# Kernel tuning notes

Measured on AMD Instinct MI355X. Metric: run time of the kernel, lower is better.

The kernel has to match this reference:

```python
import jax, jax.numpy as jnp
import numpy as np

# ---- hardware / module constants (match init_kwargs) ----
IN_BITS = 8
OUT_PREC_BITS = 8
OUT_RANGE_BITS = 4
VMAX = 0.6                      # hardware_input_vmax
I_SCALE = 8020.0                # hardware_output_current_scaling
DAC_SCALE = 1.0 / 2 ** (IN_BITS - 1)
DAC_MAX = 2 ** (IN_BITS - 1)
DAC_MIN = -DAC_MAX
ADC_SCALE = 1.0 / 2 ** OUT_PREC_BITS
ADC_MAX = 2 ** (OUT_PREC_BITS + OUT_RANGE_BITS - 1)
ADC_MIN = -ADC_MAX
BW = 1e-08
KBT = 1.380649e-23 * 300.0
E_CONST = float(np.exp(1))
V_EPS = 1e-12                   # noise_minimum_voltage
WP = 3                          # weight_precision -> L = WP-1 bit levels
L = WP - 1
MI, MO = 128, 128               # memristor tile size
TJ, TK = 2, 2                   # input/output tiling (256/128)
OUT_FEATURES = 256


def fake_quant(x, scale, qmin, qmax):
    # torch.fake_quantize_per_tensor_affine with zero_point=0 (STE grads)
    q = jnp.round(x / scale)
    y = jnp.clip(q, qmin, qmax) * scale
    mask = (q >= qmin) & (q <= qmax)
    xg = jnp.where(mask, x, jax.lax.stop_gradient(x))
    return xg + jax.lax.stop_gradient(y - xg)


def poly_eval(c, x):
    # c: [2, P] ascending-degree coeffs (pos/neg stacked), x: [B,T,I] -> [2,B,T,I]
    # Horner form: same math as sum_p c_p * x**p, grad-safe at x == 0.
    acc = jnp.broadcast_to(c[:, -1][:, None, None, None], (2,) + x.shape)
    for p in range(c.shape[-1] - 2, -1, -1):
        acc = acc * x[None] + c[:, p][:, None, None, None]
    return acc


def _paired_array(cl, ch, r, v, noise):
    # cl:[2,Pl] ch:[2,Ph] r:[2,MI,MO] v:[B,T,MI] noise:[2,T,MI,MO]
    low = poly_eval(cl, v)[..., None]       # [2,B,T,MI,1]
    high = poly_eval(ch, v)[..., None]
    r_b = r[:, None, None]                  # [2,1,1,MI,MO]
    raw = low * (1.0 - r_b) + high * r_b    # [2,B,T,MI,MO]
    johnson = 4.0 * KBT * BW * jnp.abs(raw / (jnp.abs(v)[None, ..., None] + V_EPS))
    shot = 2.0 * E_CONST * jnp.abs(raw) * BW
    sigma = jnp.sqrt(johnson + shot)
    noised = raw + noise[:, None] * sigma   # noise broadcast over batch dim B
    out = jnp.sum(noised, axis=-2)          # reduce over I -> [2,B,T,MO]
    return out[0] - out[1]                  # paired (pos - neg) bitlines


def _forward(x, poly_low, poly_high, r, bias):
    v = fake_quant(x, DAC_SCALE, DAC_MIN, DAC_MAX) * VMAX   # DAC
    B, T, _ = x.shape
    out = jnp.zeros((B, T, TK * MO), x.dtype)
    for i, bit in enumerate(reversed(range(WP - 1))):
        for j in range(TJ):
            vj = v[..., j * MI:(j + 1) * MI]
            for k in range(TK):
                nkey = jax.random.fold_in(jax.random.key(42), i * TJ * TK + j * TK + k)
                noise = jax.random.normal(nkey, (2, T, MI, MO), x.dtype)
                pair = _paired_array(poly_low[i, j, k], poly_high[i, j, k], r[i, j, k], vj, noise)
                adc_out = fake_quant(pair * I_SCALE, ADC_SCALE, ADC_MIN, ADC_MAX)  # ADC
                out = out.at[..., k * MO:(k + 1) * MO].add(adc_out * (2.0 ** bit))
    return out[..., :OUT_FEATURES] + bias


def setup_inputs() -> dict:
    key = jax.random.key(0)
    ks = jax.random.split(key, 5)
    x = jax.random.normal(ks[0], (4, 256, 256), jnp.float32)
    poly_low = jax.random.normal(ks[1], (L, TJ, TK, 2, 7), jnp.float32) * 1e-3
    poly_high = jax.random.normal(ks[2], (L, TJ, TK, 2, 6), jnp.float32) * 1e-3
    r = jax.random.uniform(ks[3], (L, TJ, TK, 2, MI, MO), dtype=jnp.float32)
    bias = jax.random.normal(ks[4], (OUT_FEATURES,), jnp.float32) * 0.01
    return {"x": x, "poly_low": poly_low, "poly_high": poly_high, "r": r, "bias": bias}


def reference(x, poly_low, poly_high, r, bias):
    return _forward(x, poly_low, poly_high, r, bias)
```

## Files before the change

### kernel.cpp

```cpp
#include <hip/hip_runtime.h>
#include <stdint.h>


struct KeyPack { uint32_t k0[8]; uint32_t k1[8]; uint32_t k2[8]; };

#define TFR(r) { x0 += x1; x1 = __builtin_amdgcn_alignbit(x1, x1, 32u - (r)); x1 ^= x0; }

__device__ __forceinline__ uint32_t tf_bits(uint32_t ks0, uint32_t ks1,
                                            uint32_t ks2, uint32_t x1) {
  uint32_t x0 = ks0;
  TFR(13) TFR(15) TFR(26) TFR(6)
  x0 += ks1; x1 += ks2 + 1u;
  TFR(17) TFR(29) TFR(16) TFR(24)
  x0 += ks2; x1 += ks0 + 2u;
  TFR(13) TFR(15) TFR(26) TFR(6)
  x0 += ks0; x1 += ks1 + 3u;
  TFR(17) TFR(29) TFR(16) TFR(24)
  x0 += ks1; x1 += ks2 + 4u;
  TFR(13) TFR(15) TFR(26) TFR(6)
  x0 += ks2; x1 += ks0 + 5u;
  return x0 ^ x1;
}

__host__ __device__ inline void threefry2x32_host(uint32_t k0, uint32_t k1,
                                                  uint32_t x0, uint32_t x1,
                                                  uint32_t& y0, uint32_t& y1) {
  const uint32_t ks0 = k0, ks1 = k1, ks2 = k0 ^ k1 ^ 0x1BD11BDAu;
  x0 += ks0; x1 += ks1;
#define TF_ROUND(r) { x0 += x1; x1 = (x1 << (r)) | (x1 >> (32 - (r))); x1 ^= x0; }
  TF_ROUND(13) TF_ROUND(15) TF_ROUND(26) TF_ROUND(6)
  x0 += ks1; x1 += ks2 + 1u;
  TF_ROUND(17) TF_ROUND(29) TF_ROUND(16) TF_ROUND(24)
  x0 += ks2; x1 += ks0 + 2u;
  TF_ROUND(13) TF_ROUND(15) TF_ROUND(26) TF_ROUND(6)
  x0 += ks0; x1 += ks1 + 3u;
  TF_ROUND(17) TF_ROUND(29) TF_ROUND(16) TF_ROUND(24)
  x0 += ks1; x1 += ks2 + 4u;
  TF_ROUND(13) TF_ROUND(15) TF_ROUND(26) TF_ROUND(6)
  x0 += ks2; x1 += ks0 + 5u;
#undef TF_ROUND
  y0 = x0; y1 = x1;
}

__device__ __forceinline__ float bits_to_normal(uint32_t bits) {
  float g = __uint_as_float(__builtin_amdgcn_alignbit(0x7Fu, bits, 9u));
  float u = fmaxf(fmaf(g, 2.0f, -3.0f), -0.99999994f);
  float w = -__logf(fmaf(u, -u, 1.0f));
  float p;
  if (w < 5.0f) {
    w -= 2.5f;
    p = (float)(2.81022636e-08 * 1.4142135623730951);
    p = fmaf(p, w, (float)( 3.43273939e-07 * 1.4142135623730951));
    p = fmaf(p, w, (float)(-3.5233877e-06  * 1.4142135623730951));
    p = fmaf(p, w, (float)(-4.39150654e-06 * 1.4142135623730951));
    p = fmaf(p, w, (float)( 0.00021858087  * 1.4142135623730951));
    p = fmaf(p, w, (float)(-0.00125372503  * 1.4142135623730951));
    p = fmaf(p, w, (float)(-0.00417768164  * 1.4142135623730951));
    p = fmaf(p, w, (float)( 0.246640727    * 1.4142135623730951));
    p = fmaf(p, w, (float)( 1.50140941     * 1.4142135623730951));
  } else {
    w = __builtin_amdgcn_sqrtf(w) - 3.0f;
    p = (float)(-0.000200214257 * 1.4142135623730951);
    p = fmaf(p, w, (float)( 0.000100950558 * 1.4142135623730951));
    p = fmaf(p, w, (float)( 0.00134934322  * 1.4142135623730951));
    p = fmaf(p, w, (float)(-0.00367342844  * 1.4142135623730951));
    p = fmaf(p, w, (float)( 0.00573950773  * 1.4142135623730951));
    p = fmaf(p, w, (float)(-0.0076224613   * 1.4142135623730951));
    p = fmaf(p, w, (float)( 0.00943887047  * 1.4142135623730951));
    p = fmaf(p, w, (float)( 1.00167406     * 1.4142135623730951));
    p = fmaf(p, w, (float)( 2.83297682     * 1.4142135623730951));
  }
  return p * u;
}

__global__ void memristor_init(const float* __restrict__ bias,
                               float* __restrict__ out) {
  int idx = blockIdx.x * 256 + threadIdx.x;
  out[idx] = bias[idx & 255];
}

__global__ __launch_bounds__(256, 4)
void memristor_main(const float* __restrict__ x,
                    const float* __restrict__ poly_low,
                    const float* __restrict__ poly_high,
                    const float* __restrict__ r,
                    float* __restrict__ out,
                    KeyPack keys) {
  __shared__ __align__(16) float LH[128][16];
  __shared__ float RED[128][9];

  const int tid = threadIdx.x;
  const int bid = blockIdx.x;
  const int c = bid >> 8;
  const int t = bid & 255;
  const int j = (c >> 1) & 1;
  const int k = c & 1;

  for (int task = tid; task < 1024; task += 256) {
    int pb = task & 7;
    int mi = task >> 3;
    int p = pb >> 2, b = pb & 3;
    float xv = x[(b * 256 + t) * 256 + j * 128 + mi];
    float q = rintf(xv * 128.0f);
    q = fminf(fmaxf(q, -128.0f), 128.0f);
    float v = (q * 0.0078125f) * 0.6f;
    const float* cl = poly_low + (c * 2 + p) * 7;
    float lo = cl[6];
    #pragma unroll
    for (int n = 5; n >= 0; --n) lo = fmaf(lo, v, cl[n]);
    const float* ch = poly_high + (c * 2 + p) * 6;
    float hi = ch[5];
    #pragma unroll
    for (int n = 4; n >= 0; --n) hi = fmaf(hi, v, ch[n]);
    LH[mi][pb] = lo;
    LH[mi][8 + pb] = hi - lo;
  }
  __syncthreads();

  const int mo = tid & 127;
  const int mih = tid >> 7;
  const int miBase = mih * 64;
  const uint32_t k0 = keys.k0[c], k1 = keys.k1[c], k2 = keys.k2[c];
  const float* r0p = r + c * 32768 + miBase * 128 + mo;
  const float* r1p = r0p + 16384;
  uint32_t sk = (uint32_t)(t * 16384 + miBase * 128 + mo) + k1;

  float acc[8];
  #pragma unroll
  for (int v2 = 0; v2 < 8; ++v2) acc[v2] = 0.0f;

  const float KS = (float)((double)((float)(2.0 * 2.718281828459045)) *
                           (double)(1e-8f));

  #pragma unroll 2
  for (int ii = 0; ii < 64; ++ii) {
    const float4* lh4 = (const float4*)(&LH[miBase + ii][0]);
    float4 L0 = lh4[0];
    float4 L1 = lh4[1];
    float4 D0 = lh4[2];
    float4 D1 = lh4[3];
    float r0 = r0p[ii * 128];
    float r1 = r1p[ii * 128];

    uint32_t b0 = tf_bits(k0, k1, k2, sk);
    uint32_t b1 = tf_bits(k0, k1, k2, sk + 4194304u);
    float n0 = bits_to_normal(b0);
    float n1 = bits_to_normal(b1);
    sk += 128u;

    float raw0 = fmaf(D0.x, r0, L0.x);
    float raw1 = fmaf(D0.y, r0, L0.y);
    float raw2 = fmaf(D0.z, r0, L0.z);
    float raw3 = fmaf(D0.w, r0, L0.w);
    float raw4 = fmaf(D1.x, r1, L1.x);
    float raw5 = fmaf(D1.y, r1, L1.y);
    float raw6 = fmaf(D1.z, r1, L1.z);
    float raw7 = fmaf(D1.w, r1, L1.w);

    float s0 = __builtin_amdgcn_sqrtf(KS * fabsf(raw0));
    float s1 = __builtin_amdgcn_sqrtf(KS * fabsf(raw1));
    float s2 = __builtin_amdgcn_sqrtf(KS * fabsf(raw2));
    float s3 = __builtin_amdgcn_sqrtf(KS * fabsf(raw3));
    float s4 = __builtin_amdgcn_sqrtf(KS * fabsf(raw4));
    float s5 = __builtin_amdgcn_sqrtf(KS * fabsf(raw5));
    float s6 = __builtin_amdgcn_sqrtf(KS * fabsf(raw6));
    float s7 = __builtin_amdgcn_sqrtf(KS * fabsf(raw7));

    acc[0] += fmaf(n0, s0, raw0);
    acc[1] += fmaf(n0, s1, raw1);
    acc[2] += fmaf(n0, s2, raw2);
    acc[3] += fmaf(n0, s3, raw3);
    acc[4] += fmaf(n1, s4, raw4);
    acc[5] += fmaf(n1, s5, raw5);
    acc[6] += fmaf(n1, s6, raw6);
    acc[7] += fmaf(n1, s7, raw7);
  }

  if (mih == 1) {
    #pragma unroll
    for (int v2 = 0; v2 < 8; ++v2) RED[mo][v2] = acc[v2];
  }
  __syncthreads();
  if (mih == 0) {
    #pragma unroll
    for (int v2 = 0; v2 < 8; ++v2) acc[v2] += RED[mo][v2];
    const float QSC = 2053120.0f;
    const float OSC = (c & 4) ? 0.00390625f : 0.0078125f;
    #pragma unroll
    for (int b = 0; b < 4; ++b) {
      float pair = acc[b] - acc[4 + b];
      float q = rintf(pair * QSC);
      q = fminf(fmaxf(q, -2048.0f), 2048.0f);
      atomicAdd(&out[(b * 256 + t) * 256 + k * 128 + mo], q * OSC);
    }
  }
}

extern "C" void kernel_launch(void* const* d_in, const int* in_sizes, int n_in,
                              void* d_out, int out_size, void* d_ws, size_t ws_size,
                              hipStream_t stream) {
  const float* x    = (const float*)d_in[0];
  const float* pl   = (const float*)d_in[1];
  const float* ph   = (const float*)d_in[2];
  const float* r    = (const float*)d_in[3];
  const float* bias = (const float*)d_in[4];
  float* out = (float*)d_out;

  KeyPack keys;
  for (uint32_t cc = 0; cc < 8; ++cc) {
    uint32_t y0, y1;
    threefry2x32_host(0u, 42u, 0u, cc, y0, y1);
    keys.k0[cc] = y0; keys.k1[cc] = y1;
    keys.k2[cc] = y0 ^ y1 ^ 0x1BD11BDAu;
  }

  memristor_init<<<1024, 256, 0, stream>>>(bias, out);
  memristor_main<<<2048, 256, 0, stream>>>(x, pl, ph, r, out, keys);
}
```

Baseline: 223.5 us.

## Pack FMAs into float2 vectors, fold threefry key injection, software-pipeline loads

Rewrites the inner loop to use two-wide float vectors so the compiler can emit packed FMA/multiply instructions on MI355X. The threefry key-injection adds are folded into the first round's addition, removing a separate add per injection. The loop is restructured to prefetch the next iteration's LDS and r values before computing the current step, to hide memory latency. The risk is higher register pressure and a wasted wraparound prefetch on the last iteration.

```diff
diff --git a/kernel.cpp b/kernel.cpp
--- a/kernel.cpp
+++ b/kernel.cpp
@@ -2,29 +2,34 @@
 #include <stdint.h>
 
 
+typedef float f32x2 __attribute__((ext_vector_type(2)));
+
 struct KeyPack { uint32_t k0[8]; uint32_t k1[8]; uint32_t k2[8]; };
 
-#define TFR(r) { x0 += x1; x1 = __builtin_amdgcn_alignbit(x1, x1, 32u - (r)); x1 ^= x0; }
+#define TFR(r)  { x0 += x1; \
+  x1 = __builtin_amdgcn_alignbit(x1, x1, 32u - (r)); x1 ^= x0; }
+#define TFR3(r, kinj) { x0 = x0 + x1 + (kinj); \
+  x1 = __builtin_amdgcn_alignbit(x1, x1, 32u - (r)); x1 ^= x0; }
 
 __device__ __forceinline__ uint32_t tf_bits(uint32_t ks0, uint32_t ks1,
                                             uint32_t ks2, uint32_t x1) {
   uint32_t x0 = ks0;
   TFR(13) TFR(15) TFR(26) TFR(6)
-  x0 += ks1; x1 += ks2 + 1u;
-  TFR(17) TFR(29) TFR(16) TFR(24)
-  x0 += ks2; x1 += ks0 + 2u;
-  TFR(13) TFR(15) TFR(26) TFR(6)
-  x0 += ks0; x1 += ks1 + 3u;
-  TFR(17) TFR(29) TFR(16) TFR(24)
-  x0 += ks1; x1 += ks2 + 4u;
-  TFR(13) TFR(15) TFR(26) TFR(6)
+  x1 += ks2 + 1u;
+  TFR3(17, ks1) TFR(29) TFR(16) TFR(24)
+  x1 += ks0 + 2u;
+  TFR3(13, ks2) TFR(15) TFR(26) TFR(6)
+  x1 += ks1 + 3u;
+  TFR3(17, ks0) TFR(29) TFR(16) TFR(24)
+  x1 += ks2 + 4u;
+  TFR3(13, ks1) TFR(15) TFR(26) TFR(6)
   x0 += ks2; x1 += ks0 + 5u;
   return x0 ^ x1;
 }
 
-__host__ __device__ inline void threefry2x32_host(uint32_t k0, uint32_t k1,
-                                                  uint32_t x0, uint32_t x1,
-                                                  uint32_t& y0, uint32_t& y1) {
+__host__ inline void threefry2x32_host(uint32_t k0, uint32_t k1,
+                                       uint32_t x0, uint32_t x1,
+                                       uint32_t& y0, uint32_t& y1) {
   const uint32_t ks0 = k0, ks1 = k1, ks2 = k0 ^ k1 ^ 0x1BD11BDAu;
   x0 += ks0; x1 += ks1;
 #define TF_ROUND(r) { x0 += x1; x1 = (x1 << (r)) | (x1 >> (32 - (r))); x1 ^= x0; }
@@ -125,71 +130,87 @@
   const float* r1p = r0p + 16384;
   uint32_t sk = (uint32_t)(t * 16384 + miBase * 128 + mo) + k1;
 
-  float acc[8];
-  #pragma unroll
-  for (int v2 = 0; v2 < 8; ++v2) acc[v2] = 0.0f;
+  f32x2 acc01 = {0.f, 0.f}, acc23 = {0.f, 0.f};
+  f32x2 acc45 = {0.f, 0.f}, acc67 = {0.f, 0.f};
 
   const float KS = (float)((double)((float)(2.0 * 2.718281828459045)) *
                            (double)(1e-8f));
-
-  #pragma unroll 2
-  for (int ii = 0; ii < 64; ++ii) {
-    const float4* lh4 = (const float4*)(&LH[miBase + ii][0]);
-    float4 L0 = lh4[0];
-    float4 L1 = lh4[1];
-    float4 D0 = lh4[2];
-    float4 D1 = lh4[3];
-    float r0 = r0p[ii * 128];
-    float r1 = r1p[ii * 128];
-
+  const f32x2 KSv = {KS, KS};
+
+  auto STEP = [&](float4 F0, float4 F1, float4 F2, float4 F3,
+                  float rr0, float rr1) {
     uint32_t b0 = tf_bits(k0, k1, k2, sk);
     uint32_t b1 = tf_bits(k0, k1, k2, sk + 4194304u);
+    sk += 128u;
     float n0 = bits_to_normal(b0);
     float n1 = bits_to_normal(b1);
-    sk += 128u;
-
-    float raw0 = fmaf(D0.x, r0, L0.x);
-    float raw1 = fmaf(D0.y, r0, L0.y);
-    float raw2 = fmaf(D0.z, r0, L0.z);
-    float raw3 = fmaf(D0.w, r0, L0.w);
-    float raw4 = fmaf(D1.x, r1, L1.x);
-    float raw5 = fmaf(D1.y, r1, L1.y);
-    float raw6 = fmaf(D1.z, r1, L1.z);
-    float raw7 = fmaf(D1.w, r1, L1.w);
-
-    float s0 = __builtin_amdgcn_sqrtf(KS * fabsf(raw0));
-    float s1 = __builtin_amdgcn_sqrtf(KS * fabsf(raw1));
-    float s2 = __builtin_amdgcn_sqrtf(KS * fabsf(raw2));
-    float s3 = __builtin_amdgcn_sqrtf(KS * fabsf(raw3));
-    float s4 = __builtin_amdgcn_sqrtf(KS * fabsf(raw4));
-    float s5 = __builtin_amdgcn_sqrtf(KS * fabsf(raw5));
-    float s6 = __builtin_amdgcn_sqrtf(KS * fabsf(raw6));
-    float s7 = __builtin_amdgcn_sqrtf(KS * fabsf(raw7));
-
-    acc[0] += fmaf(n0, s0, raw0);
-    acc[1] += fmaf(n0, s1, raw1);
-    acc[2] += fmaf(n0, s2, raw2);
-    acc[3] += fmaf(n0, s3, raw3);
-    acc[4] += fmaf(n1, s4, raw4);
-    acc[5] += fmaf(n1, s5, raw5);
-    acc[6] += fmaf(n1, s6, raw6);
-    acc[7] += fmaf(n1, s7, raw7);
+    f32x2 rv0 = {rr0, rr0}, rv1 = {rr1, rr1};
+    f32x2 n0v = {n0, n0},   n1v = {n1, n1};
+
+    f32x2 raw01 = __builtin_elementwise_fma((f32x2){F2.x, F2.y}, rv0, (f32x2){F0.x, F0.y});
+    f32x2 raw23 = __builtin_elementwise_fma((f32x2){F2.z, F2.w}, rv0, (f32x2){F0.z, F0.w});
+    f32x2 raw45 = __builtin_elementwise_fma((f32x2){F3.x, F3.y}, rv1, (f32x2){F1.x, F1.y});
+    f32x2 raw67 = __builtin_elementwise_fma((f32x2){F3.z, F3.w}, rv1, (f32x2){F1.z, F1.w});
+
+    f32x2 kr01 = raw01 * KSv, kr23 = raw23 * KSv;
+    f32x2 kr45 = raw45 * KSv, kr67 = raw67 * KSv;
+    f32x2 s01 = { __builtin_amdgcn_sqrtf(fabsf(kr01.x)),
+                  __builtin_amdgcn_sqrtf(fabsf(kr01.y)) };
+    f32x2 s23 = { __builtin_amdgcn_sqrtf(fabsf(kr23.x)),
+                  __builtin_amdgcn_sqrtf(fabsf(kr23.y)) };
+    f32x2 s45 = { __builtin_amdgcn_sqrtf(fabsf(kr45.x)),
+                  __builtin_amdgcn_sqrtf(fabsf(kr45.y)) };
+    f32x2 s67 = { __builtin_amdgcn_sqrtf(fabsf(kr67.x)),
+                  __builtin_amdgcn_sqrtf(fabsf(kr67.y)) };
+
+    acc01 += __builtin_elementwise_fma(n0v, s01, raw01);
+    acc23 += __builtin_elementwise_fma(n0v, s23, raw23);
+    acc45 += __builtin_elementwise_fma(n1v, s45, raw45);
+    acc67 += __builtin_elementwise_fma(n1v, s67, raw67);
+  };
+
+  float4 a0, a1, a2, a3; float ra0, ra1;
+  {
+    const float4* lh = (const float4*)&LH[miBase][0];
+    a0 = lh[0]; a1 = lh[1]; a2 = lh[2]; a3 = lh[3];
+    ra0 = r0p[0]; ra1 = r1p[0];
+  }
+
+  #pragma unroll 1
+  for (int ii = 0; ii < 64; ii += 2) {
+    const float4* lhB = (const float4*)&LH[miBase + ii + 1][0];
+    float4 bb0 = lhB[0], bb1 = lhB[1], bb2 = lhB[2], bb3 = lhB[3];
+    float rb0 = r0p[(ii + 1) * 128];
+    float rb1 = r1p[(ii + 1) * 128];
+    STEP(a0, a1, a2, a3, ra0, ra1);
+
+    int nx = (ii + 2) & 63;
+    const float4* lhA = (const float4*)&LH[miBase + nx][0];
+    a0 = lhA[0]; a1 = lhA[1]; a2 = lhA[2]; a3 = lhA[3];
+    ra0 = r0p[nx * 128];
+    ra1 = r1p[nx * 128];
+    STEP(bb0, bb1, bb2, bb3, rb0, rb1);
   }
 
   if (mih == 1) {
-    #pragma unroll
-    for (int v2 = 0; v2 < 8; ++v2) RED[mo][v2] = acc[v2];
+    RED[mo][0] = acc01.x; RED[mo][1] = acc01.y;
+    RED[mo][2] = acc23.x; RED[mo][3] = acc23.y;
+    RED[mo][4] = acc45.x; RED[mo][5] = acc45.y;
+    RED[mo][6] = acc67.x; RED[mo][7] = acc67.y;
   }
   __syncthreads();
   if (mih == 0) {
-    #pragma unroll
-    for (int v2 = 0; v2 < 8; ++v2) acc[v2] += RED[mo][v2];
+    acc01.x += RED[mo][0]; acc01.y += RED[mo][1];
+    acc23.x += RED[mo][2]; acc23.y += RED[mo][3];
+    acc45.x += RED[mo][4]; acc45.y += RED[mo][5];
+    acc67.x += RED[mo][6]; acc67.y += RED[mo][7];
     const float QSC = 2053120.0f;
     const float OSC = (c & 4) ? 0.00390625f : 0.0078125f;
+    float pair[4] = { acc01.x - acc45.x, acc01.y - acc45.y,
+                      acc23.x - acc67.x, acc23.y - acc67.y };
     #pragma unroll
     for (int b = 0; b < 4; ++b) {
-      float pair = acc[b] - acc[4 + b];
-      float q = rintf(pair * QSC);
+      float q = rintf(pair[b] * QSC);
       q = fminf(fmaxf(q, -2048.0f), 2048.0f);
       atomicAdd(&out[(b * 256 + t) * 256 + k * 128 + mo], q * OSC);
     }
```

Measured after the change: 231.3 us. 3.5% more time.
